# Kernel optimization log

Hardware: AMD Instinct MI355X
Metric: run time of the kernel (lower is better)

## Reference

```python
import jax, jax.numpy as jnp
import numpy as np

# Config mirrors init_kwargs
B, C, K, D = 32768, 100, 8, 512
ROUTING_T = 0.07      # routing_temperature
PRIOR_T = 0.07        # class_prior_temperature
SUB_T = 0.05          # subproto_temperature
RIDGE = 0.1           # ridge (fixed mode)
EPS = 1e-8            # input_norm_eps
PROTO_INIT_SCALE = 0.02


def _l2norm(x, eps=EPS):
    # F.normalize(p=2, dim=-1, eps=eps)
    n = jnp.linalg.norm(x, axis=-1, keepdims=True)
    return x / jnp.maximum(n, eps)


def setup_inputs() -> dict:
    key = jax.random.key(0)
    k1, k2 = jax.random.split(key)
    h = jax.random.normal(k1, (B, D), dtype=jnp.float32)
    # learned parameter: prototypes [num_classes, protos_per_class, feature_dim]
    prototypes = jax.random.normal(k2, (C, K, D), dtype=jnp.float32) * PROTO_INIT_SCALE
    return {"h": h, "prototypes": prototypes}


def reference(h, prototypes):
    # ---- input normalization (input_norm_mode='l2_hypersphere') ----
    hn = _l2norm(h)                                   # [B, D]
    Pn = _l2norm(prototypes)                          # [C, K, D]

    # ---- prototype-distance routing (cosine sims, multiple temperatures) ----
    cos = jnp.einsum('bd,ckd->bck', hn, Pn)           # [B, C, K]
    w_sub = jax.nn.softmax(cos / SUB_T, axis=-1)      # subproto routing weights
    class_sim = jnp.sum(w_sub * cos, axis=-1)         # pooled aggregation [B, C]
    prior_logits = class_sim / PRIOR_T                # class prior logits

    # ---- per-class closed-form ridge solve (same_opp_balanced support) ----
    # Support for class c: its K sub-prototypes (target +1, total weight 0.5)
    # vs. the other C-1 class centers (target -1, total weight 0.5).
    centers = _l2norm(jnp.mean(Pn, axis=1))           # [C, D] pooled class centers
    ws = 0.5 / K
    wo = 0.5 / (C - 1)

    # Gram of same-class support, batched over classes: [C, D, D]
    G_same = ws * jnp.einsum('ckd,cke->cde', Pn, Pn)
    # Opp gram = all-centers gram minus own center outer product
    S_all = centers.T @ centers                       # [D, D]
    G_opp = wo * (S_all[None, :, :] - jnp.einsum('cd,ce->cde', centers, centers))
    A = G_same + G_opp + RIDGE * jnp.eye(D, dtype=h.dtype)  # [C, D, D]

    # RHS X^T S y: +1 on same protos, -1 on opp centers
    b_same = ws * jnp.sum(Pn, axis=1)                 # [C, D]
    csum = jnp.sum(centers, axis=0)                   # [D]
    b_opp = -wo * (csum[None, :] - centers)           # [C, D]
    b = b_same + b_opp

    W = jnp.linalg.solve(A, b[..., None])[..., 0]     # [C, D] per-class ridge weights

    # ---- residual head: routed closed-form logits added to prior ----
    residual = (hn @ W.T) / ROUTING_T                 # [B, C]
    return prior_logits + residual
```

## Files before the change

### kernel.cpp

```cpp
#include <hip/hip_runtime.h>
#include <math.h>

#define NB 32768
#define NC 100
#define NK 8
#define ND 512
#define ALPHA 22.0f
#define NEU_ITERS 12

typedef __attribute__((ext_vector_type(8))) short short8;
typedef __attribute__((ext_vector_type(4))) float f32x4;

__device__ __forceinline__ void gl_lds16(const void* g, void* l) {
    __builtin_amdgcn_global_load_lds(
        (const __attribute__((address_space(1))) void*)g,
        (__attribute__((address_space(3))) void*)l, 16, 0, 0);
}

__device__ __forceinline__ float warpReduceSum(float v) {
#pragma unroll
    for (int off = 32; off > 0; off >>= 1) v += __shfl_xor(v, off);
    return v;
}

__device__ float blockReduceSum256(float v, float* red) {
    int tid = threadIdx.x;
    v = warpReduceSum(v);
    __syncthreads();
    if ((tid & 63) == 0) red[tid >> 6] = v;
    __syncthreads();
    return red[0] + red[1] + red[2] + red[3];
}

__device__ __forceinline__ unsigned short f2bf(float x) {
    unsigned u = __float_as_uint(x);
    u = (u + 0x7FFFu + ((u >> 16) & 1u)) >> 16;
    return (unsigned short)u;
}
__device__ __forceinline__ float bf2f(unsigned short h) {
    return __uint_as_float(((unsigned)h) << 16);
}


__global__ void k_prep_class(const float* __restrict__ protos, float* __restrict__ X,
                             float* __restrict__ centersT) {
    __shared__ float red[4];
    int c = blockIdx.x;
    int tid = threadIdx.x;
    const float eps = 1e-8f;
    float pv0[NK], pv1[NK];
#pragma unroll
    for (int k = 0; k < NK; ++k) {
        pv0[k] = protos[(c * NK + k) * ND + tid];
        pv1[k] = protos[(c * NK + k) * ND + tid + 256];
    }
    float sv0 = 0.f, sv1 = 0.f;
#pragma unroll
    for (int k = 0; k < NK; ++k) {
        float ss = blockReduceSum256(pv0[k] * pv0[k] + pv1[k] * pv1[k], red);
        float inv = 1.0f / fmaxf(sqrtf(ss), eps);
        pv0[k] *= inv; pv1[k] *= inv;
        X[(c * NK + k) * ND + tid] = pv0[k];
        X[(c * NK + k) * ND + tid + 256] = pv1[k];
        sv0 += pv0[k]; sv1 += pv1[k];
    }
    float ssum = blockReduceSum256(sv0 * sv0 + sv1 * sv1, red);
    float mnorm = sqrtf(ssum) * 0.125f;
    float cinv = 0.125f / fmaxf(mnorm, eps);
    float* centers = X + 800 * ND;
    float c0 = sv0 * cinv, c1 = sv1 * cinv;
    centers[c * ND + tid] = c0;
    centers[c * ND + tid + 256] = c1;
    centersT[tid * NC + c] = c0;
    centersT[(tid + 256) * NC + c] = c1;
    const float ws = 0.5f / 8.0f;
    float* bvec = X + 900 * ND;
    bvec[c * ND + tid] = ws * sv0;
    bvec[c * ND + tid + 256] = ws * sv1;
}

__global__ void k_csum(const float* __restrict__ X, float* __restrict__ csum) {
    int d = blockIdx.x * blockDim.x + threadIdx.x;
    const float* centers = X + 800 * ND;
    float s = 0.f;
    for (int c = 0; c < NC; ++c) s += centers[c * ND + d];
    csum[d] = s;
}

__global__ void k_bopp(float* __restrict__ X, const float* __restrict__ csum) {
    int c = blockIdx.x, tid = threadIdx.x;
    const float wo = 0.5f / 99.0f;
    const float* centers = X + 800 * ND;
    float* bvec = X + 900 * ND;
    for (int d = tid; d < ND; d += 256)
        bvec[c * ND + d] -= wo * (csum[d] - centers[c * ND + d]);
}

__global__ void k_gram(const float* __restrict__ X, const float* __restrict__ centersT,
                       float* __restrict__ M) {
    __shared__ float cs[ND];
    int i = blockIdx.x, tid = threadIdx.x;
    const float* centers = X + 800 * ND;
    for (int d = tid; d < ND; d += 128) cs[d] = centers[i * ND + d];
    __syncthreads();
    if (tid < NC) {
        float s = 0.f;
#pragma unroll 8
        for (int d = 0; d < ND; ++d) s += cs[d] * centersT[d * NC + tid];
        float ahat = s + ((tid == i) ? (0.1f * 99.0f / 0.5f) : 0.f);
        M[i * NC + tid] = ((tid == i) ? 1.f : 0.f) - ahat * (1.0f / ALPHA);
    }
}

__global__ void k_T1(const float* __restrict__ X, const float* __restrict__ centersT,
                     float* __restrict__ T1) {
    __shared__ float xs[ND];
    int j = blockIdx.x, tid = threadIdx.x;
    reinterpret_cast<float4*>(xs)[tid] = reinterpret_cast<const float4*>(X + j * ND)[tid];
    __syncthreads();
    if (tid < NC) {
        float s = 0.f;
#pragma unroll 8
        for (int d = 0; d < ND; ++d) s += xs[d] * centersT[d * NC + tid];
        T1[j * NC + tid] = s;
    }
}

__global__ __launch_bounds__(256) void k_T2neu(const float* __restrict__ M,
                                               const float* __restrict__ T1,
                                               float* __restrict__ T2) {
    __shared__ float Msh[NC * 108];
    __shared__ float pbuf[2][4][104];
    int tid = threadIdx.x;
    int wave = tid >> 6, lane = tid & 63;
    int j = blockIdx.x * 4 + wave;
    for (int idx = tid; idx < NC * NC; idx += 256) {
        int i = idx / NC, m = idx - i * NC;
        Msh[i * 108 + m] = M[idx];
    }
    int i0 = lane;
    int i1 = lane + 64;
    int i1c = (i1 < NC) ? i1 : 0;
    float t0 = T1[j * NC + i0];
    float t1v = (i1 < NC) ? T1[j * NC + i1] : 0.f;
    float s0 = t0, s1 = t1v;
    pbuf[0][wave][i0] = t0;
    if (i1 < NC) pbuf[0][wave][i1] = t1v;
    __syncthreads();
    int cur = 0;
    for (int it = 0; it < NEU_ITERS; ++it) {
        const float* p = pbuf[cur][wave];
        float y0 = 0.f, y1 = 0.f;
#pragma unroll 5
        for (int m = 0; m < NC; m += 4) {
            float4 pv = *reinterpret_cast<const float4*>(p + m);
            float4 a0 = *reinterpret_cast<const float4*>(&Msh[i0 * 108 + m]);
            float4 a1 = *reinterpret_cast<const float4*>(&Msh[i1c * 108 + m]);
            y0 = fmaf(a0.x, pv.x, y0); y0 = fmaf(a0.y, pv.y, y0);
            y0 = fmaf(a0.z, pv.z, y0); y0 = fmaf(a0.w, pv.w, y0);
            y1 = fmaf(a1.x, pv.x, y1); y1 = fmaf(a1.y, pv.y, y1);
            y1 = fmaf(a1.z, pv.z, y1); y1 = fmaf(a1.w, pv.w, y1);
        }
        s0 += y0; s1 += y1;
        int nxt = cur ^ 1;
        pbuf[nxt][wave][i0] = y0;
        if (i1 < NC) pbuf[nxt][wave][i1] = y1;
        cur = nxt;
    }
    T2[j * NC + i0] = s0 * (1.0f / ALPHA);
    if (i1 < NC) T2[j * NC + i1] = s1 * (1.0f / ALPHA);
}

__global__ void k_Y(const float* __restrict__ X, const float* __restrict__ T2,
                    float* __restrict__ Y) {
    __shared__ float t2s[NC];
    int j = blockIdx.x, tid = threadIdx.x;
    for (int i = tid; i < NC; i += 256) t2s[i] = T2[j * NC + i];
    __syncthreads();
    const float* centers = X + 800 * ND;
    for (int d = tid; d < ND; d += 256) {
        float s = 0.f;
        for (int i = 0; i < NC; ++i) s += centers[i * ND + d] * t2s[i];
        Y[j * ND + d] = (X[j * ND + d] - s) * 10.0f;
    }
}

__global__ void k_solve(const float* __restrict__ X, const float* __restrict__ Y,
                        float* __restrict__ W) {
    __shared__ float Vs[9 * 516];
    __shared__ float Ys[10 * 516];
    __shared__ float SL[9 * 10];
    __shared__ float zL[9];
    int c = blockIdx.x, tid = threadIdx.x;
    for (int idx = tid; idx < 9 * 128; idx += 256) {
        int a = idx >> 7, q = idx & 127;
        int row = (a < 8) ? (c * 8 + a) : (800 + c);
        reinterpret_cast<float4*>(&Vs[a * 516])[q] =
            reinterpret_cast<const float4*>(X + row * ND)[q];
    }
    for (int idx = tid; idx < 10 * 128; idx += 256) {
        int a = idx >> 7, q = idx & 127;
        int row = (a < 8) ? (c * 8 + a) : ((a == 8) ? (800 + c) : (900 + c));
        reinterpret_cast<float4*>(&Ys[a * 516])[q] =
            reinterpret_cast<const float4*>(Y + row * ND)[q];
    }
    __syncthreads();
    if (tid < 90) {
        int a = tid / 10, bb = tid - (tid / 10) * 10;
        float s = 0.f;
        for (int d = 0; d < ND; ++d) s += Vs[a * 516 + d] * Ys[bb * 516 + d];
        if (bb == a) s += 16.0f;
        if (bb == a && a == 8) s += -198.0f - 16.0f;
        SL[tid] = s;
    }
    __syncthreads();
    if (tid == 0) {
        for (int p = 0; p < 9; ++p) {
            int best = p; float bv = fabsf(SL[p * 10 + p]);
            for (int r = p + 1; r < 9; ++r) {
                float v = fabsf(SL[r * 10 + p]);
                if (v > bv) { bv = v; best = r; }
            }
            if (best != p)
                for (int j = p; j < 10; ++j) {
                    float t = SL[p * 10 + j]; SL[p * 10 + j] = SL[best * 10 + j]; SL[best * 10 + j] = t;
                }
            float ip = 1.0f / SL[p * 10 + p];
            for (int r = p + 1; r < 9; ++r) {
                float f = SL[r * 10 + p] * ip;
                for (int j = p; j < 10; ++j) SL[r * 10 + j] -= f * SL[p * 10 + j];
            }
        }
        for (int p = 8; p >= 0; --p) {
            float s = SL[p * 10 + 9];
            for (int j = p + 1; j < 9; ++j) s -= SL[p * 10 + j] * zL[j];
            zL[p] = s / SL[p * 10 + p];
        }
    }
    __syncthreads();
    for (int d = tid; d < ND; d += 256) {
        float w = Ys[9 * 516 + d];
#pragma unroll
        for (int a = 0; a < 9; ++a) w -= zL[a] * Ys[a * 516 + d];
        W[c * ND + d] = w;
    }
}


__global__ void k_hn(const float* __restrict__ h, unsigned short* __restrict__ hnb) {
    int tid = threadIdx.x;
    int wave = tid >> 6, lane = tid & 63;
    int r = blockIdx.x * 4 + wave;
    const float4* hp = reinterpret_cast<const float4*>(h + (size_t)r * ND);
    float4 v0 = hp[lane * 2];
    float4 v1 = hp[lane * 2 + 1];
    float s = v0.x * v0.x + v0.y * v0.y + v0.z * v0.z + v0.w * v0.w
            + v1.x * v1.x + v1.y * v1.y + v1.z * v1.z + v1.w * v1.w;
    s = warpReduceSum(s);
    float inv = 1.0f / fmaxf(sqrtf(s), 1e-8f);
    uint4 o;
    o.x = (unsigned)f2bf(v0.x * inv) | ((unsigned)f2bf(v0.y * inv) << 16);
    o.y = (unsigned)f2bf(v0.z * inv) | ((unsigned)f2bf(v0.w * inv) << 16);
    o.z = (unsigned)f2bf(v1.x * inv) | ((unsigned)f2bf(v1.y * inv) << 16);
    o.w = (unsigned)f2bf(v1.z * inv) | ((unsigned)f2bf(v1.w * inv) << 16);
    reinterpret_cast<uint4*>(hnb + (size_t)r * ND)[lane] = o;
}

__global__ void k_packB(const float* __restrict__ X, const float* __restrict__ W,
                        unsigned short* __restrict__ Bp) {
    int tid = threadIdx.x;
    int row = blockIdx.x * 4 + (tid >> 6);
    int lane = tid & 63;
    int c = row / 10, j = row - c * 10;
    float vals[8];
    if (c >= NC) {
#pragma unroll
        for (int q = 0; q < 8; ++q) vals[q] = 0.f;
    } else if (j < 8) {
        const float* src = X + (size_t)(c * 8 + j) * ND + lane * 8;
#pragma unroll
        for (int q = 0; q < 8; ++q) vals[q] = src[q];
    } else {
        const float* src = W + (size_t)c * ND + lane * 8;
#pragma unroll
        for (int q = 0; q < 8; ++q) {
            float w = src[q];
            vals[q] = (j == 8) ? w : (w - bf2f(f2bf(w)));
        }
    }
    uint4 o;
    o.x = (unsigned)f2bf(vals[0]) | ((unsigned)f2bf(vals[1]) << 16);
    o.y = (unsigned)f2bf(vals[2]) | ((unsigned)f2bf(vals[3]) << 16);
    o.z = (unsigned)f2bf(vals[4]) | ((unsigned)f2bf(vals[5]) << 16);
    o.w = (unsigned)f2bf(vals[6]) | ((unsigned)f2bf(vals[7]) << 16);
    reinterpret_cast<uint4*>(Bp + (size_t)row * ND)[lane] = o;
}


__global__ __launch_bounds__(256, 3) void k_main_mfma(
        const unsigned short* __restrict__ hnb, const unsigned short* __restrict__ Bp,
        float* __restrict__ out) {
    __shared__ __align__(16) char smem[41728];
    unsigned short* As = (unsigned short*)smem;
    unsigned short* Bs = (unsigned short*)smem + 8192;
    float* Cs = (float*)smem;

    int tid = threadIdx.x;
    int wave = tid >> 6, lane = tid & 63;
    int m = lane & 15, g = lane >> 4;
    int rs = m & 7;
    int rowhalf = wave & 1, colhalf = wave >> 1;
    int cb = blockIdx.x;
    int r0 = blockIdx.y * 128;

    int rsub = lane >> 3;
    int osw = (lane & 7) ^ rsub;

    f32x4 acc[4][5] = {};

    for (int kc = 0; kc < 8; ++kc) {
        __syncthreads();
#pragma unroll
        for (int q = 0; q < 4; ++q) {
            int ch = wave * 4 + q;
            const unsigned short* gp =
                hnb + (size_t)(r0 + ch * 8 + rsub) * ND + kc * 64 + osw * 8;
            gl_lds16(gp, As + ch * 512);
        }
#pragma unroll
        for (int q = 0; q < 5; ++q) {
            int ch = wave * 5 + q;
            const unsigned short* gp =
                Bp + (size_t)(cb * 160 + ch * 8 + rsub) * ND + kc * 64 + osw * 8;
            gl_lds16(gp, Bs + ch * 512);
        }
        __syncthreads();
#pragma unroll
        for (int kk = 0; kk < 2; ++kk) {
            short8 af[4], bfr[5];
#pragma unroll
            for (int rt = 0; rt < 4; ++rt)
                af[rt] = *reinterpret_cast<const short8*>(
                    As + (rowhalf * 64 + rt * 16 + m) * 64 + (((kk << 2) + g) ^ rs) * 8);
#pragma unroll
            for (int ct = 0; ct < 5; ++ct)
                bfr[ct] = *reinterpret_cast<const short8*>(
                    Bs + (colhalf * 80 + ct * 16 + m) * 64 + (((kk << 2) + g) ^ rs) * 8);
#pragma unroll
            for (int rt = 0; rt < 4; ++rt)
#pragma unroll
                for (int ct = 0; ct < 5; ++ct)
                    acc[rt][ct] = __builtin_amdgcn_mfma_f32_16x16x32_bf16(
                        af[rt], bfr[ct], acc[rt][ct], 0, 0, 0);
        }
    }

    for (int p = 0; p < 2; ++p) {
        __syncthreads();
        if (rowhalf == p) {
#pragma unroll
            for (int rt = 0; rt < 4; ++rt)
#pragma unroll
                for (int ct = 0; ct < 5; ++ct)
#pragma unroll
                    for (int reg = 0; reg < 4; ++reg) {
                        int lr = rt * 16 + g * 4 + reg;
                        int lc = colhalf * 80 + ct * 16 + m;
                        Cs[lr * 163 + lc] = acc[rt][ct][reg];
                    }
        }
        __syncthreads();
        {
            int cl = tid & 15;
            int c = cb * 16 + cl;
#pragma unroll
            for (int q = 0; q < 4; ++q) {
                int r = (tid >> 4) + q * 16;
                float v[10];
#pragma unroll
                for (int j = 0; j < 10; ++j) v[j] = Cs[r * 163 + cl * 10 + j];
                float mx = v[0];
#pragma unroll
                for (int j = 1; j < 8; ++j) mx = fmaxf(mx, v[j]);
                float se = 0.f, sec = 0.f;
#pragma unroll
                for (int j = 0; j < 8; ++j) {
                    float e = __expf((v[j] - mx) * 20.0f);
                    se += e; sec += e * v[j];
                }
                float res = v[8] + v[9];
                if (c < NC)
                    out[(size_t)(r0 + p * 64 + r) * NC + c] =
                        (sec / se + res) * (1.0f / 0.07f);
            }
        }
    }
}

extern "C" void kernel_launch(void* const* d_in, const int* in_sizes, int n_in,
                              void* d_out, int out_size, void* d_ws, size_t ws_size,
                              hipStream_t stream) {
    (void)in_sizes; (void)n_in; (void)out_size; (void)ws_size;
    const float* h = (const float*)d_in[0];
    const float* protos = (const float*)d_in[1];
    float* out = (float*)d_out;
    float* ws = (float*)d_ws;

    float* X        = ws;
    float* csum     = X + 512000;
    float* M        = csum + 512;
    float* T1       = M + 10000;
    float* T2       = T1 + 100000;
    float* Y        = T2 + 100000;
    float* W        = Y + 512000;
    float* centersT = W + 51200;
    unsigned short* hnb = (unsigned short*)(centersT + 51200);
    unsigned short* Bp  = hnb + (size_t)NB * ND;

    k_hn<<<NB / 4, 256, 0, stream>>>(h, hnb);
    k_prep_class<<<NC, 256, 0, stream>>>(protos, X, centersT);
    k_csum<<<2, 256, 0, stream>>>(X, csum);
    k_bopp<<<NC, 256, 0, stream>>>(X, csum);
    k_gram<<<NC, 128, 0, stream>>>(X, centersT, M);
    k_T1<<<1000, 128, 0, stream>>>(X, centersT, T1);
    k_T2neu<<<250, 256, 0, stream>>>(M, T1, T2);
    k_Y<<<1000, 256, 0, stream>>>(X, T2, Y);
    k_solve<<<NC, 256, 0, stream>>>(X, Y, W);
    k_packB<<<280, 256, 0, stream>>>(X, W, Bp);
    dim3 grid(7, NB / 128);
    k_main_mfma<<<grid, 256, 0, stream>>>(hnb, Bp, out);
}
```

Measured before the change: 278.7 us.

## Fuse setup kernels, solve via low-rank algebra, double-buffer main MFMA GEMM

Merges csum and b_opp into one kernel, and folds the gram matrix M into a wave-per-row T1 kernel. Replaces the Y and solve kernels with a 10x10 reformulation built from T1 and T2, and writes bf16 Bp directly, which removes k_packB. The main MFMA kernel moves to 64-row tiles with double-buffered LDS prefetch and an XCD-aware block swizzle. The aim is to cut launch count and intermediate traffic and to overlap loads with MFMA, at the cost of lower occupancy (launch bounds 2) and more LDS.

```diff
diff --git a/kernel.cpp b/kernel.cpp
--- a/kernel.cpp
+++ b/kernel.cpp
@@ -43,7 +43,7 @@
 
 
 __global__ void k_prep_class(const float* __restrict__ protos, float* __restrict__ X,
-                             float* __restrict__ centersT) {
+                             float* __restrict__ centersT, unsigned short* __restrict__ Bp) {
     __shared__ float red[4];
     int c = blockIdx.x;
     int tid = threadIdx.x;
@@ -62,6 +62,8 @@
         pv0[k] *= inv; pv1[k] *= inv;
         X[(c * NK + k) * ND + tid] = pv0[k];
         X[(c * NK + k) * ND + tid + 256] = pv1[k];
+        Bp[(size_t)(c * 10 + k) * ND + tid] = f2bf(pv0[k]);
+        Bp[(size_t)(c * 10 + k) * ND + tid + 256] = f2bf(pv1[k]);
         sv0 += pv0[k]; sv1 += pv1[k];
     }
     float ssum = blockReduceSum256(sv0 * sv0 + sv1 * sv1, red);
@@ -79,50 +81,52 @@
     bvec[c * ND + tid + 256] = ws * sv1;
 }
 
-__global__ void k_csum(const float* __restrict__ X, float* __restrict__ csum) {
-    int d = blockIdx.x * blockDim.x + threadIdx.x;
-    const float* centers = X + 800 * ND;
-    float s = 0.f;
-    for (int c = 0; c < NC; ++c) s += centers[c * ND + d];
-    csum[d] = s;
-}
-
-__global__ void k_bopp(float* __restrict__ X, const float* __restrict__ csum) {
+__global__ void k_csbopp(float* __restrict__ X) {
     int c = blockIdx.x, tid = threadIdx.x;
     const float wo = 0.5f / 99.0f;
     const float* centers = X + 800 * ND;
     float* bvec = X + 900 * ND;
-    for (int d = tid; d < ND; d += 256)
-        bvec[c * ND + d] -= wo * (csum[d] - centers[c * ND + d]);
-}
-
-__global__ void k_gram(const float* __restrict__ X, const float* __restrict__ centersT,
-                       float* __restrict__ M) {
-    __shared__ float cs[ND];
-    int i = blockIdx.x, tid = threadIdx.x;
-    const float* centers = X + 800 * ND;
-    for (int d = tid; d < ND; d += 128) cs[d] = centers[i * ND + d];
-    __syncthreads();
-    if (tid < NC) {
+#pragma unroll
+    for (int h = 0; h < 2; ++h) {
+        int d = tid + h * 256;
         float s = 0.f;
+#pragma unroll 4
+        for (int i = 0; i < NC; ++i) s += centers[i * ND + d];
+        bvec[c * ND + d] -= wo * (s - centers[c * ND + d]);
+    }
+}
+
+__global__ __launch_bounds__(256) void k_T1M(const float* __restrict__ X,
+                                             const float* __restrict__ centersT,
+                                             float* __restrict__ T1, float* __restrict__ M) {
+    __shared__ float xs[4][ND];
+    int tid = threadIdx.x;
+    int wave = tid >> 6, lane = tid & 63;
+    int j = blockIdx.x * 4 + wave;
+    reinterpret_cast<float4*>(xs[wave])[lane * 2] =
+        reinterpret_cast<const float4*>(X + (size_t)j * ND)[lane * 2];
+    reinterpret_cast<float4*>(xs[wave])[lane * 2 + 1] =
+        reinterpret_cast<const float4*>(X + (size_t)j * ND)[lane * 2 + 1];
+    __syncthreads();
+    int i0 = lane, i1 = lane + 64;
+    int i1c = (i1 < NC) ? i1 : 0;
+    float s0 = 0.f, s1 = 0.f;
 #pragma unroll 8
-        for (int d = 0; d < ND; ++d) s += cs[d] * centersT[d * NC + tid];
-        float ahat = s + ((tid == i) ? (0.1f * 99.0f / 0.5f) : 0.f);
-        M[i * NC + tid] = ((tid == i) ? 1.f : 0.f) - ahat * (1.0f / ALPHA);
-    }
-}
-
-__global__ void k_T1(const float* __restrict__ X, const float* __restrict__ centersT,
-                     float* __restrict__ T1) {
-    __shared__ float xs[ND];
-    int j = blockIdx.x, tid = threadIdx.x;
-    reinterpret_cast<float4*>(xs)[tid] = reinterpret_cast<const float4*>(X + j * ND)[tid];
-    __syncthreads();
-    if (tid < NC) {
-        float s = 0.f;
-#pragma unroll 8
-        for (int d = 0; d < ND; ++d) s += xs[d] * centersT[d * NC + tid];
-        T1[j * NC + tid] = s;
+    for (int d = 0; d < ND; ++d) {
+        float xv = xs[wave][d];
+        s0 = fmaf(xv, centersT[d * NC + i0], s0);
+        s1 = fmaf(xv, centersT[d * NC + i1c], s1);
+    }
+    T1[j * NC + i0] = s0;
+    if (i1 < NC) T1[j * NC + i1] = s1;
+    if (j >= 800 && j < 900) {
+        int ci = j - 800;
+        float a0 = s0 + ((i0 == ci) ? 19.8f : 0.f);
+        M[ci * NC + i0] = ((i0 == ci) ? 1.f : 0.f) - a0 * (1.0f / ALPHA);
+        if (i1 < NC) {
+            float a1 = s1 + ((i1 == ci) ? 19.8f : 0.f);
+            M[ci * NC + i1] = ((i1 == ci) ? 1.f : 0.f) - a1 * (1.0f / ALPHA);
+        }
     }
 }
 
@@ -171,47 +175,52 @@
     if (i1 < NC) T2[j * NC + i1] = s1 * (1.0f / ALPHA);
 }
 
-__global__ void k_Y(const float* __restrict__ X, const float* __restrict__ T2,
-                    float* __restrict__ Y) {
-    __shared__ float t2s[NC];
-    int j = blockIdx.x, tid = threadIdx.x;
-    for (int i = tid; i < NC; i += 256) t2s[i] = T2[j * NC + i];
-    __syncthreads();
-    const float* centers = X + 800 * ND;
-    for (int d = tid; d < ND; d += 256) {
-        float s = 0.f;
-        for (int i = 0; i < NC; ++i) s += centers[i * ND + d] * t2s[i];
-        Y[j * ND + d] = (X[j * ND + d] - s) * 10.0f;
-    }
-}
-
-__global__ void k_solve(const float* __restrict__ X, const float* __restrict__ Y,
-                        float* __restrict__ W) {
-    __shared__ float Vs[9 * 516];
-    __shared__ float Ys[10 * 516];
+__global__ __launch_bounds__(256) void k_solveW(const float* __restrict__ X,
+                                                const float* __restrict__ T1,
+                                                const float* __restrict__ T2,
+                                                unsigned short* __restrict__ Bp) {
+    int c = blockIdx.x, tid = threadIdx.x;
+    if (c >= NC) {
+        uint4 z = {0, 0, 0, 0};
+        for (int idx = tid; idx < 10 * ND / 8; idx += 256)
+            reinterpret_cast<uint4*>(Bp + (size_t)c * 10 * ND)[idx] = z;
+        return;
+    }
+    __shared__ float Xs[10 * 516];
+    __shared__ float T1s[10 * 104];
+    __shared__ float T2s[10 * 104];
+    __shared__ float G[10][10];
     __shared__ float SL[9 * 10];
     __shared__ float zL[9];
-    int c = blockIdx.x, tid = threadIdx.x;
-    for (int idx = tid; idx < 9 * 128; idx += 256) {
-        int a = idx >> 7, q = idx & 127;
-        int row = (a < 8) ? (c * 8 + a) : (800 + c);
-        reinterpret_cast<float4*>(&Vs[a * 516])[q] =
-            reinterpret_cast<const float4*>(X + row * ND)[q];
-    }
+    __shared__ float q[104];
     for (int idx = tid; idx < 10 * 128; idx += 256) {
-        int a = idx >> 7, q = idx & 127;
+        int a = idx >> 7, p = idx & 127;
         int row = (a < 8) ? (c * 8 + a) : ((a == 8) ? (800 + c) : (900 + c));
-        reinterpret_cast<float4*>(&Ys[a * 516])[q] =
-            reinterpret_cast<const float4*>(Y + row * ND)[q];
+        reinterpret_cast<float4*>(&Xs[a * 516])[p] =
+            reinterpret_cast<const float4*>(X + (size_t)row * ND)[p];
+    }
+    for (int idx = tid; idx < 10 * NC; idx += 256) {
+        int a = idx / NC, i = idx - a * NC;
+        int row = (a < 8) ? (c * 8 + a) : ((a == 8) ? (800 + c) : (900 + c));
+        T1s[a * 104 + i] = T1[row * NC + i];
+        T2s[a * 104 + i] = T2[row * NC + i];
+    }
+    __syncthreads();
+    if (tid < 100) {
+        int a = tid / 10, b = tid - (tid / 10) * 10;
+        float s = 0.f;
+        for (int d = 0; d < ND; ++d) s += Xs[a * 516 + d] * Xs[b * 516 + d];
+        G[a][b] = s;
     }
     __syncthreads();
     if (tid < 90) {
-        int a = tid / 10, bb = tid - (tid / 10) * 10;
+        int a = tid / 10, b = tid - (tid / 10) * 10;
         float s = 0.f;
-        for (int d = 0; d < ND; ++d) s += Vs[a * 516 + d] * Ys[bb * 516 + d];
-        if (bb == a) s += 16.0f;
-        if (bb == a && a == 8) s += -198.0f - 16.0f;
-        SL[tid] = s;
+#pragma unroll 4
+        for (int i = 0; i < NC; ++i) s += T1s[a * 104 + i] * T2s[b * 104 + i];
+        float val = (G[a][b] - s) * 10.0f;
+        if (b == a) val += (a < 8) ? 16.0f : -198.0f;
+        SL[tid] = val;
     }
     __syncthreads();
     if (tid == 0) {
@@ -238,11 +247,27 @@
         }
     }
     __syncthreads();
-    for (int d = tid; d < ND; d += 256) {
-        float w = Ys[9 * 516 + d];
-#pragma unroll
-        for (int a = 0; a < 9; ++a) w -= zL[a] * Ys[a * 516 + d];
-        W[c * ND + d] = w;
+    if (tid < NC) {
+        float s = T2s[9 * 104 + tid];
+#pragma unroll
+        for (int a = 0; a < 9; ++a) s -= zL[a] * T2s[a * 104 + tid];
+        q[tid] = s;
+    }
+    __syncthreads();
+    const float* centers = X + 800 * ND;
+#pragma unroll
+    for (int h = 0; h < 2; ++h) {
+        int d = tid + h * 256;
+        float u = Xs[9 * 516 + d];
+#pragma unroll
+        for (int a = 0; a < 9; ++a) u -= zL[a] * Xs[a * 516 + d];
+        float s = 0.f;
+#pragma unroll 4
+        for (int i = 0; i < NC; ++i) s = fmaf(centers[i * ND + d], q[i], s);
+        float w = (u - s) * 10.0f;
+        unsigned short hi = f2bf(w);
+        Bp[(size_t)(c * 10 + 8) * ND + d] = hi;
+        Bp[(size_t)(c * 10 + 9) * ND + d] = f2bf(w - bf2f(hi));
     }
 }
 
@@ -266,88 +291,67 @@
     reinterpret_cast<uint4*>(hnb + (size_t)r * ND)[lane] = o;
 }
 
-__global__ void k_packB(const float* __restrict__ X, const float* __restrict__ W,
-                        unsigned short* __restrict__ Bp) {
-    int tid = threadIdx.x;
-    int row = blockIdx.x * 4 + (tid >> 6);
-    int lane = tid & 63;
-    int c = row / 10, j = row - c * 10;
-    float vals[8];
-    if (c >= NC) {
-#pragma unroll
-        for (int q = 0; q < 8; ++q) vals[q] = 0.f;
-    } else if (j < 8) {
-        const float* src = X + (size_t)(c * 8 + j) * ND + lane * 8;
-#pragma unroll
-        for (int q = 0; q < 8; ++q) vals[q] = src[q];
-    } else {
-        const float* src = W + (size_t)c * ND + lane * 8;
-#pragma unroll
-        for (int q = 0; q < 8; ++q) {
-            float w = src[q];
-            vals[q] = (j == 8) ? w : (w - bf2f(f2bf(w)));
-        }
-    }
-    uint4 o;
-    o.x = (unsigned)f2bf(vals[0]) | ((unsigned)f2bf(vals[1]) << 16);
-    o.y = (unsigned)f2bf(vals[2]) | ((unsigned)f2bf(vals[3]) << 16);
-    o.z = (unsigned)f2bf(vals[4]) | ((unsigned)f2bf(vals[5]) << 16);
-    o.w = (unsigned)f2bf(vals[6]) | ((unsigned)f2bf(vals[7]) << 16);
-    reinterpret_cast<uint4*>(Bp + (size_t)row * ND)[lane] = o;
-}
-
-
-__global__ __launch_bounds__(256, 3) void k_main_mfma(
+
+__global__ __launch_bounds__(256, 2) void k_main_mfma(
         const unsigned short* __restrict__ hnb, const unsigned short* __restrict__ Bp,
         float* __restrict__ out) {
-    __shared__ __align__(16) char smem[41728];
-    unsigned short* As = (unsigned short*)smem;
-    unsigned short* Bs = (unsigned short*)smem + 8192;
+    __shared__ __align__(16) char smem[57344];
     float* Cs = (float*)smem;
 
     int tid = threadIdx.x;
     int wave = tid >> 6, lane = tid & 63;
     int m = lane & 15, g = lane >> 4;
     int rs = m & 7;
-    int rowhalf = wave & 1, colhalf = wave >> 1;
-    int cb = blockIdx.x;
-    int r0 = blockIdx.y * 128;
+    int rh = wave & 1, ch = wave >> 1;
+
+    int id = blockIdx.x;
+    int xcd = id & 7, kk2 = id >> 3;
+    int cb = kk2 % 7;
+    int rb = (kk2 / 7) * 8 + xcd;
+    int r0 = rb * 64;
 
     int rsub = lane >> 3;
     int osw = (lane & 7) ^ rsub;
 
-    f32x4 acc[4][5] = {};
-
+    f32x4 acc[2][5] = {};
+
+    auto issue = [&](int kc, int p) {
+        unsigned short* As = (unsigned short*)(smem + p * 28672);
+        unsigned short* Bs = As + 4096;
+#pragma unroll
+        for (int q2 = 0; q2 < 2; ++q2) {
+            int chk = wave * 2 + q2;
+            gl_lds16(hnb + (size_t)(r0 + chk * 8 + rsub) * ND + kc * 64 + osw * 8,
+                     As + chk * 512);
+        }
+#pragma unroll
+        for (int q2 = 0; q2 < 5; ++q2) {
+            int chk = wave * 5 + q2;
+            gl_lds16(Bp + (size_t)(cb * 160 + chk * 8 + rsub) * ND + kc * 64 + osw * 8,
+                     Bs + chk * 512);
+        }
+    };
+
+    issue(0, 0);
     for (int kc = 0; kc < 8; ++kc) {
+        int cur = kc & 1;
         __syncthreads();
-#pragma unroll
-        for (int q = 0; q < 4; ++q) {
-            int ch = wave * 4 + q;
-            const unsigned short* gp =
-                hnb + (size_t)(r0 + ch * 8 + rsub) * ND + kc * 64 + osw * 8;
-            gl_lds16(gp, As + ch * 512);
-        }
-#pragma unroll
-        for (int q = 0; q < 5; ++q) {
-            int ch = wave * 5 + q;
-            const unsigned short* gp =
-                Bp + (size_t)(cb * 160 + ch * 8 + rsub) * ND + kc * 64 + osw * 8;
-            gl_lds16(gp, Bs + ch * 512);
-        }
-        __syncthreads();
+        if (kc < 7) issue(kc + 1, cur ^ 1);
+        unsigned short* As = (unsigned short*)(smem + cur * 28672);
+        unsigned short* Bs = As + 4096;
 #pragma unroll
         for (int kk = 0; kk < 2; ++kk) {
-            short8 af[4], bfr[5];
-#pragma unroll
-            for (int rt = 0; rt < 4; ++rt)
+            short8 af[2], bfr[5];
+#pragma unroll
+            for (int rt = 0; rt < 2; ++rt)
                 af[rt] = *reinterpret_cast<const short8*>(
-                    As + (rowhalf * 64 + rt * 16 + m) * 64 + (((kk << 2) + g) ^ rs) * 8);
+                    As + (rh * 32 + rt * 16 + m) * 64 + (((kk << 2) + g) ^ rs) * 8);
 #pragma unroll
             for (int ct = 0; ct < 5; ++ct)
                 bfr[ct] = *reinterpret_cast<const short8*>(
-                    Bs + (colhalf * 80 + ct * 16 + m) * 64 + (((kk << 2) + g) ^ rs) * 8);
-#pragma unroll
-            for (int rt = 0; rt < 4; ++rt)
+                    Bs + (ch * 80 + ct * 16 + m) * 64 + (((kk << 2) + g) ^ rs) * 8);
+#pragma unroll
+            for (int rt = 0; rt < 2; ++rt)
 #pragma unroll
                 for (int ct = 0; ct < 5; ++ct)
                     acc[rt][ct] = __builtin_amdgcn_mfma_f32_16x16x32_bf16(
@@ -355,44 +359,39 @@
         }
     }
 
-    for (int p = 0; p < 2; ++p) {
-        __syncthreads();
-        if (rowhalf == p) {
-#pragma unroll
-            for (int rt = 0; rt < 4; ++rt)
-#pragma unroll
-                for (int ct = 0; ct < 5; ++ct)
-#pragma unroll
-                    for (int reg = 0; reg < 4; ++reg) {
-                        int lr = rt * 16 + g * 4 + reg;
-                        int lc = colhalf * 80 + ct * 16 + m;
-                        Cs[lr * 163 + lc] = acc[rt][ct][reg];
-                    }
-        }
-        __syncthreads();
-        {
-            int cl = tid & 15;
-            int c = cb * 16 + cl;
-#pragma unroll
-            for (int q = 0; q < 4; ++q) {
-                int r = (tid >> 4) + q * 16;
-                float v[10];
-#pragma unroll
-                for (int j = 0; j < 10; ++j) v[j] = Cs[r * 163 + cl * 10 + j];
-                float mx = v[0];
-#pragma unroll
-                for (int j = 1; j < 8; ++j) mx = fmaxf(mx, v[j]);
-                float se = 0.f, sec = 0.f;
-#pragma unroll
-                for (int j = 0; j < 8; ++j) {
-                    float e = __expf((v[j] - mx) * 20.0f);
-                    se += e; sec += e * v[j];
-                }
-                float res = v[8] + v[9];
-                if (c < NC)
-                    out[(size_t)(r0 + p * 64 + r) * NC + c] =
-                        (sec / se + res) * (1.0f / 0.07f);
+    __syncthreads();
+#pragma unroll
+    for (int rt = 0; rt < 2; ++rt)
+#pragma unroll
+        for (int ct = 0; ct < 5; ++ct)
+#pragma unroll
+            for (int reg = 0; reg < 4; ++reg) {
+                int lr = rh * 32 + rt * 16 + g * 4 + reg;
+                int lc = ch * 80 + ct * 16 + m;
+                Cs[lr * 163 + lc] = acc[rt][ct][reg];
             }
+    __syncthreads();
+    {
+        int cl = tid & 15;
+        int c = cb * 16 + cl;
+#pragma unroll
+        for (int q2 = 0; q2 < 4; ++q2) {
+            int r = (tid >> 4) + q2 * 16;
+            float v[10];
+#pragma unroll
+            for (int j = 0; j < 10; ++j) v[j] = Cs[r * 163 + cl * 10 + j];
+            float mx = v[0];
+#pragma unroll
+            for (int j = 1; j < 8; ++j) mx = fmaxf(mx, v[j]);
+            float se = 0.f, sec = 0.f;
+#pragma unroll
+            for (int j = 0; j < 8; ++j) {
+                float e = __expf((v[j] - mx) * 20.0f);
+                se += e; sec += e * v[j];
+            }
+            float res = v[8] + v[9];
+            if (c < NC)
+                out[(size_t)(r0 + r) * NC + c] = (sec / se + res) * (1.0f / 0.07f);
         }
     }
 }
@@ -407,26 +406,18 @@
     float* ws = (float*)d_ws;
 
     float* X        = ws;
-    float* csum     = X + 512000;
-    float* M        = csum + 512;
+    float* centersT = X + 512000;
+    float* M        = centersT + 51200;
     float* T1       = M + 10000;
     float* T2       = T1 + 100000;
-    float* Y        = T2 + 100000;
-    float* W        = Y + 512000;
-    float* centersT = W + 51200;
-    unsigned short* hnb = (unsigned short*)(centersT + 51200);
+    unsigned short* hnb = (unsigned short*)(T2 + 100000);
     unsigned short* Bp  = hnb + (size_t)NB * ND;
 
     k_hn<<<NB / 4, 256, 0, stream>>>(h, hnb);
-    k_prep_class<<<NC, 256, 0, stream>>>(protos, X, centersT);
-    k_csum<<<2, 256, 0, stream>>>(X, csum);
-    k_bopp<<<NC, 256, 0, stream>>>(X, csum);
-    k_gram<<<NC, 128, 0, stream>>>(X, centersT, M);
-    k_T1<<<1000, 128, 0, stream>>>(X, centersT, T1);
+    k_prep_class<<<NC, 256, 0, stream>>>(protos, X, centersT, Bp);
+    k_csbopp<<<NC, 256, 0, stream>>>(X);
+    k_T1M<<<250, 256, 0, stream>>>(X, centersT, T1, M);
     k_T2neu<<<250, 256, 0, stream>>>(M, T1, T2);
-    k_Y<<<1000, 256, 0, stream>>>(X, T2, Y);
-    k_solve<<<NC, 256, 0, stream>>>(X, Y, W);
-    k_packB<<<280, 256, 0, stream>>>(X, W, Bp);
-    dim3 grid(7, NB / 128);
-    k_main_mfma<<<grid, 256, 0, stream>>>(hnb, Bp, out);
-}
+    k_solveW<<<112, 256, 0, stream>>>(X, T1, T2, Bp);
+    k_main_mfma<<<3584, 256, 0, stream>>>(hnb, Bp, out);
+}
```

Result: faster. 241.3 us (-13.4%).
